# Performance work log

Hardware: AMD Instinct MI355X
Metric: run time of the kernel (lower is better)

The kernel has to match this reference:

```python
import jax, jax.numpy as jnp
import numpy as np

N = 50000      # nodes
E = 400000     # edges
IN = 128       # in_channels
C = 32         # out_channels per head
H1 = 8         # heads layer 1
MSG = 64       # msg_dim
TD = 64        # time encoder out_channels
ED = MSG + TD  # edge_dim = 128
HID = H1 * C   # 256


def _lin(k, fi, fo):
    return jax.random.normal(k, (fi, fo), jnp.float32) / np.float32(np.sqrt(fi))


def setup_inputs() -> dict:
    key = jax.random.key(0)
    ks = jax.random.split(key, 32)
    inp = {
        'x': jax.random.normal(ks[0], (N, IN), jnp.float32),
        'last_update': jax.random.uniform(ks[1], (N,), jnp.float32) * 1000.0,
        'edge_index': jax.random.randint(ks[2], (2, E), 0, N, jnp.int64),
        't': jax.random.uniform(ks[3], (E,), jnp.float32) * 1000.0,
        'msg': jax.random.normal(ks[4], (E, MSG), jnp.float32),
        # time encoder: Linear(1, TD) then cos
        'tw': jax.random.normal(ks[5], (TD,), jnp.float32),
        'tb': jnp.zeros((TD,), jnp.float32),
        # layer 1: TransformerConv(IN, C, heads=8, concat=True, edge_dim=ED)
        'Wq1': _lin(ks[6], IN, HID), 'bq1': jnp.zeros((HID,), jnp.float32),
        'Wk1': _lin(ks[7], IN, HID), 'bk1': jnp.zeros((HID,), jnp.float32),
        'Wv1': _lin(ks[8], IN, HID), 'bv1': jnp.zeros((HID,), jnp.float32),
        'We1': _lin(ks[9], ED, HID),                       # lin_edge, no bias
        'Ws1': _lin(ks[10], IN, HID), 'bs1': jnp.zeros((HID,), jnp.float32),
        # layer 2: TransformerConv(HID, C, heads=1, concat=False, edge_dim=ED)
        'Wq2': _lin(ks[11], HID, C), 'bq2': jnp.zeros((C,), jnp.float32),
        'Wk2': _lin(ks[12], HID, C), 'bk2': jnp.zeros((C,), jnp.float32),
        'Wv2': _lin(ks[13], HID, C), 'bv2': jnp.zeros((C,), jnp.float32),
        'We2': _lin(ks[14], ED, C),
        'Ws2': _lin(ks[15], HID, C), 'bs2': jnp.zeros((C,), jnp.float32),
    }
    return inp


def _seg_softmax(logits, seg, n):
    # numerically-stable softmax over variable-size neighborhoods (per dst node)
    m = jax.ops.segment_max(logits, seg, num_segments=n)
    m = jnp.where(jnp.isfinite(m), m, 0.0)
    e = jnp.exp(logits - jax.lax.stop_gradient(m)[seg])
    s = jax.ops.segment_sum(e, seg, num_segments=n)
    return e / (s[seg] + 1e-16)


def _transformer_conv(x, edge_attr, src, dst, Wq, bq, Wk, bk, Wv, bv, We, Ws, bs, heads, ch, concat):
    n = x.shape[0]
    q = (x @ Wq + bq).reshape(n, heads, ch)[dst]          # (E,H,C) gather at dst
    k = ((x @ Wk + bk)[src]).reshape(-1, heads, ch)       # (E,H,C) gather at src
    v = ((x @ Wv + bv)[src]).reshape(-1, heads, ch)
    e = (edge_attr @ We).reshape(-1, heads, ch)
    k = k + e
    alpha = (q * k).sum(-1) / np.float32(np.sqrt(ch))     # (E,H)
    alpha = _seg_softmax(alpha, dst, n)
    out = jax.ops.segment_sum(alpha[..., None] * (v + e), dst, num_segments=n)  # (N,H,C)
    out = out.reshape(n, heads * ch) if concat else out.mean(axis=1)
    return out + x @ Ws + bs                               # root/skip connection


def reference(x, last_update, edge_index, t, msg, tw, tb,
              Wq1, bq1, Wk1, bk1, Wv1, bv1, We1, Ws1, bs1,
              Wq2, bq2, Wk2, bk2, Wv2, bv2, We2, Ws2, bs2):
    src, dst = edge_index[0], edge_index[1]
    rel_t = last_update[src] - t                          # (E,)
    rel_enc = jnp.cos(rel_t[:, None] * tw[None, :] + tb)  # TGN time encoding (E,TD)
    edge_attr = jnp.concatenate([rel_enc, msg], axis=-1)  # (E,ED)
    h = jax.nn.relu(_transformer_conv(x, edge_attr, src, dst,
                                      Wq1, bq1, Wk1, bk1, Wv1, bv1, We1, Ws1, bs1,
                                      H1, C, True))
    out = jax.nn.relu(_transformer_conv(h, edge_attr, src, dst,
                                        Wq2, bq2, Wk2, bk2, Wv2, bv2, We2, Ws2, bs2,
                                        1, C, False))
    return out
```

## Files before the change

kernel.cpp:

```cpp
#include <hip/hip_runtime.h>
#include <math.h>

#define NN 50000
#define NE 400000
#define RSQRT32 0.17677669529663687f

typedef __attribute__((ext_vector_type(8))) short bf16x8;
typedef __attribute__((ext_vector_type(4))) float f32x4;
#define MFMA_B16(a, b, c) __builtin_amdgcn_mfma_f32_16x16x32_bf16(a, b, c, 0, 0, 0)

#define O_FLAG  0ULL
#define O_BSUM  256ULL
#define O_SRCI  1280ULL
#define O_DSTI  (O_SRCI + 1600000ULL)
#define O_DEG   (O_DSTI + 1600000ULL)
#define O_CUR   (O_DEG + 200192ULL)
#define O_START (O_CUR + 200192ULL)
#define O_SRCS  (O_START + 200704ULL)
#define O_ORIG  (O_SRCS + 1600000ULL)
#define O_RELT  (O_ORIG + 1600000ULL)
#define O_Q1    (O_RELT + 1600000ULL)
#define O_K1    (O_Q1 + 25600000ULL)
#define O_V1    (O_K1 + 25600000ULL)
#define O_S1M   (O_V1 + 25600000ULL)
#define O_G1    (O_S1M + 25600000ULL)
#define O_WB1   (O_G1 + 102400000ULL)
#define O_WG1   (O_WB1 + 262144ULL)
#define O_WF1   (O_WG1 + 65536ULL)
#define O_WB2   (O_WF1 + 65536ULL)
#define O_NUMV1 (O_WB2 + 65536ULL)
#define WS_TOTAL (O_NUMV1 + 51200000ULL)
#define O_S1    O_DSTI
#define O_A1    O_G1
#define O_H     O_V1
#define O_Q2    O_Q1
#define O_K2    (O_Q1 + 6400000ULL)
#define O_V2    (O_Q1 + 12800000ULL)
#define O_S2M   (O_Q1 + 19200000ULL)
#define O_G2    O_K1
#define O_A2    O_S1M
#define O_NUMV2 O_G1
#define O_S2    O_CUR

__device__ __forceinline__ unsigned short f2bf(float f) {
    unsigned int u = __float_as_uint(f);
    unsigned int r = (u + 0x7fffu + ((u >> 16) & 1u)) >> 16;
    return (unsigned short)r;
}
__device__ __forceinline__ float bf2f(unsigned short u) {
    return __uint_as_float(((unsigned int)u) << 16);
}
__device__ __forceinline__ float4 ld_bf16x4(const unsigned short* p) {
    const ushort4 u = *(const ushort4*)p;
    float4 r;
    r.x = bf2f(u.x); r.y = bf2f(u.y); r.z = bf2f(u.z); r.w = bf2f(u.w);
    return r;
}
__device__ __forceinline__ ushort4 st_bf16x4(float a, float b, float c, float d) {
    ushort4 u; u.x = f2bf(a); u.y = f2bf(b); u.z = f2bf(c); u.w = f2bf(d);
    return u;
}

__global__ void k_detect(const unsigned int* ei, int* flag) {
    if (threadIdx.x == 0) {
        int is64 = 1;
        for (int i = 0; i < 64; ++i)
            if (ei[2 * i + 1] != 0u) { is64 = 0; break; }
        *flag = is64;
    }
}

__global__ void k_convhist(const void* ei, const int* flag,
                           int* __restrict__ srcI, int* __restrict__ dstI,
                           int* __restrict__ deg) {
    int i = blockIdx.x * 256 + threadIdx.x;
    if (i >= NE) return;
    int s, d;
    if (*flag) {
        const long long* p = (const long long*)ei;
        s = (int)p[i]; d = (int)p[NE + i];
    } else {
        const int* p = (const int*)ei;
        s = p[i]; d = p[NE + i];
    }
    srcI[i] = s;
    dstI[i] = d;
    atomicAdd(&deg[d], 1);
}

__global__ void k_scanA(const int* __restrict__ deg, int* __restrict__ locs,
                        int* __restrict__ bsum) {
    __shared__ int sm[256];
    const int t = threadIdx.x;
    const int gidx = blockIdx.x * 256 + t;
    int v = (gidx < NN) ? deg[gidx] : 0;
    sm[t] = v;
    __syncthreads();
    for (int off = 1; off < 256; off <<= 1) {
        int u = (t >= off) ? sm[t - off] : 0;
        __syncthreads();
        sm[t] += u;
        __syncthreads();
    }
    if (gidx < NN) locs[gidx] = sm[t];
    if (t == 255) bsum[blockIdx.x] = sm[255];
}

__global__ void k_scanB(int* __restrict__ bsum) {
    __shared__ int sm[256];
    const int t = threadIdx.x;
    int v = (t < 196) ? bsum[t] : 0;
    sm[t] = v;
    __syncthreads();
    for (int off = 1; off < 256; off <<= 1) {
        int u = (t >= off) ? sm[t - off] : 0;
        __syncthreads();
        sm[t] += u;
        __syncthreads();
    }
    if (t < 196) bsum[t] = sm[t] - v;
}

__global__ void k_scanC(const int* __restrict__ deg, const int* __restrict__ bsum,
                        int* __restrict__ startA, int* __restrict__ cursor) {
    const int t = threadIdx.x;
    const int gidx = blockIdx.x * 256 + t;
    if (gidx < NN) {
        const int ex = startA[gidx] - deg[gidx] + bsum[blockIdx.x];
        startA[gidx] = ex;
        cursor[gidx] = ex;
    }
    if (gidx == 0) startA[NN] = NE;
}

__global__ void k_scatter(const int* __restrict__ srcI, const int* __restrict__ dstI,
                          const float* __restrict__ lu, const float* __restrict__ tE,
                          int* __restrict__ cursor,
                          int* __restrict__ srcS, int* __restrict__ orig,
                          float* __restrict__ relT) {
    int i = blockIdx.x * 256 + threadIdx.x;
    if (i >= NE) return;
    const int d = dstI[i];
    const int s = srcI[i];
    const int pos = atomicAdd(&cursor[d], 1);
    srcS[pos] = s;
    orig[pos] = i;
    relT[pos] = lu[s] - tE[i];
}

__global__ void k_prepw(
    const float* __restrict__ Wq1, const float* __restrict__ Wk1,
    const float* __restrict__ Wv1, const float* __restrict__ Ws1,
    const float* __restrict__ We1,
    const float* __restrict__ Wq2, const float* __restrict__ Wk2,
    const float* __restrict__ Wv2, const float* __restrict__ Ws2,
    unsigned short* __restrict__ WB1, unsigned short* __restrict__ WG1,
    unsigned short* __restrict__ WF1, unsigned short* __restrict__ WB2)
{
    const int i = blockIdx.x * 256 + threadIdx.x;
    if (i < 131072) {
        const int part = i >> 15;
        const int rem = i & 32767;
        const int n = rem >> 7, k = rem & 127;
        const float* W = part == 0 ? Wq1 : part == 1 ? Wk1 : part == 2 ? Wv1 : Ws1;
        WB1[i] = f2bf(W[(size_t)k * 256 + n]);
    } else if (i < 163840) {
        const int j = i - 131072;
        const int h = j >> 12, ko = (j >> 5) & 127, c = j & 31;
        WG1[j] = f2bf(We1[(size_t)ko * 256 + h * 32 + c]);
    } else if (i < 196608) {
        const int j = i - 163840;
        const int h = j >> 12, c = (j >> 7) & 31, ko = j & 127;
        WF1[j] = f2bf(We1[(size_t)ko * 256 + h * 32 + c]);
    } else if (i < 229376) {
        const int j = i - 196608;
        const int col = j >> 8, k = j & 255;
        const int part = col >> 5, pc = col & 31;
        const float* W = part == 0 ? Wq2 : part == 1 ? Wk2 : part == 2 ? Wv2 : Ws2;
        WB2[j] = f2bf(W[(size_t)k * 32 + pc]);
    }
}

__global__ __launch_bounds__(256) void k_gemm1m(
    const float* __restrict__ x, const unsigned short* __restrict__ WB1,
    const float* __restrict__ c0, const float* __restrict__ c1,
    const float* __restrict__ c2, const float* __restrict__ c3,
    unsigned short* __restrict__ Q1b, unsigned short* __restrict__ K1b,
    unsigned short* __restrict__ V1b, unsigned short* __restrict__ S1mb)
{
    __shared__ unsigned short As[64 * 136];
    __shared__ unsigned short Bs[64 * 136];
    const int t = threadIdx.x;
    const int row0 = blockIdx.x * 64;
    const int by = blockIdx.y;
    const int part = by >> 2;
    const int pcol0 = (by & 3) * 64;
    const float* bp = part == 0 ? c0 : part == 1 ? c1 : part == 2 ? c2 : c3;
    unsigned short* Ob = part == 0 ? Q1b : part == 1 ? K1b : part == 2 ? V1b : S1mb;

    {
        const int r = t >> 2, cc = (t & 3) * 32;
        const int gr = row0 + r;
        unsigned short* dst = As + r * 136 + cc;
        if (gr < NN) {
            const float4* xp = (const float4*)(x + (size_t)gr * 128 + cc);
            #pragma unroll
            for (int i = 0; i < 8; ++i) {
                const float4 v = xp[i];
                *(ushort4*)(dst + 4 * i) = st_bf16x4(v.x, v.y, v.z, v.w);
            }
        } else {
            const ushort4 z = {0, 0, 0, 0};
            #pragma unroll
            for (int i = 0; i < 8; ++i) *(ushort4*)(dst + 4 * i) = z;
        }
    }
    {
        const int n = t >> 2, kk = (t & 3) * 32;
        const unsigned short* src = WB1 + ((size_t)part * 256 + pcol0 + n) * 128 + kk;
        unsigned short* dst = Bs + n * 136 + kk;
        #pragma unroll
        for (int i = 0; i < 4; ++i)
            *(bf16x8*)(dst + 8 * i) = *(const bf16x8*)(src + 8 * i);
    }
    __syncthreads();

    const int w = t >> 6, lane = t & 63, m = lane & 15, quad = lane >> 4;
    f32x4 acc[4];
    #pragma unroll
    for (int i = 0; i < 4; ++i) acc[i] = (f32x4){0.f, 0.f, 0.f, 0.f};
    #pragma unroll
    for (int kc = 0; kc < 4; ++kc) {
        const bf16x8 af = *(const bf16x8*)(As + (16 * w + m) * 136 + kc * 32 + quad * 8);
        #pragma unroll
        for (int ct = 0; ct < 4; ++ct) {
            const bf16x8 bf = *(const bf16x8*)(Bs + (16 * ct + m) * 136 + kc * 32 + quad * 8);
            acc[ct] = MFMA_B16(af, bf, acc[ct]);
        }
    }
    #pragma unroll
    for (int ct = 0; ct < 4; ++ct) {
        const int colp = pcol0 + ct * 16 + m;
        const float b = bp[colp];
        #pragma unroll
        for (int r = 0; r < 4; ++r) {
            const int gr = row0 + 16 * w + quad * 4 + r;
            if (gr < NN) Ob[(size_t)gr * 256 + colp] = f2bf(acc[ct][r] + b);
        }
    }
}

__global__ __launch_bounds__(256) void k_g1m(
    const unsigned short* __restrict__ Q1b, const unsigned short* __restrict__ WG1,
    unsigned short* __restrict__ G1b)
{
    __shared__ unsigned short As[64 * 40];
    __shared__ unsigned short Bs[128 * 40];
    const int t = threadIdx.x;
    const int n0 = blockIdx.x * 64;
    const int h = blockIdx.y;
    {
        const int n = t >> 2, c = (t & 3) * 8;
        const int gn = n0 + n;
        bf16x8 v = {};
        if (gn < NN) v = *(const bf16x8*)(Q1b + (size_t)gn * 256 + h * 32 + c);
        *(bf16x8*)(As + n * 40 + c) = v;
    }
    {
        const int ko = t >> 1, c = (t & 1) * 16;
        const unsigned short* src = WG1 + (size_t)h * 4096 + ko * 32 + c;
        *(bf16x8*)(Bs + ko * 40 + c) = *(const bf16x8*)(src);
        *(bf16x8*)(Bs + ko * 40 + c + 8) = *(const bf16x8*)(src + 8);
    }
    __syncthreads();

    const int w = t >> 6, lane = t & 63, m = lane & 15, quad = lane >> 4;
    f32x4 acc[8];
    #pragma unroll
    for (int i = 0; i < 8; ++i) acc[i] = (f32x4){0.f, 0.f, 0.f, 0.f};
    const bf16x8 af = *(const bf16x8*)(As + (16 * w + m) * 40 + quad * 8);
    #pragma unroll
    for (int ct = 0; ct < 8; ++ct) {
        const bf16x8 bf = *(const bf16x8*)(Bs + (16 * ct + m) * 40 + quad * 8);
        acc[ct] = MFMA_B16(af, bf, acc[ct]);
    }
    #pragma unroll
    for (int ct = 0; ct < 8; ++ct) {
        const int k = ct * 16 + m;
        #pragma unroll
        for (int r = 0; r < 4; ++r) {
            const int gn = n0 + 16 * w + quad * 4 + r;
            if (gn < NN) G1b[(size_t)gn * 1024 + h * 128 + k] = f2bf(acc[ct][r]);
        }
    }
}

__global__ __launch_bounds__(256) void k_g2(
    const float* __restrict__ Q2, const float* __restrict__ We2,
    float* __restrict__ G2)
{
    __shared__ float Qs[64][36];
    __shared__ float Ws[128][36];
    const int t = threadIdx.x;
    const int n0 = blockIdx.x * 64;
    {
        const int n = t >> 2, c8 = (t & 3) * 8;
        float4 v0 = make_float4(0.f,0.f,0.f,0.f), v1 = v0;
        if (n0 + n < NN) {
            v0 = *(const float4*)(Q2 + (size_t)(n0 + n) * 32 + c8);
            v1 = *(const float4*)(Q2 + (size_t)(n0 + n) * 32 + c8 + 4);
        }
        *(float4*)(&Qs[n][c8]) = v0;
        *(float4*)(&Qs[n][c8 + 4]) = v1;
    }
    {
        const int k = t >> 1, c16 = (t & 1) * 16;
        #pragma unroll
        for (int i = 0; i < 4; ++i)
            *(float4*)(&Ws[k][c16 + 4 * i]) =
                *(const float4*)(We2 + (size_t)k * 32 + c16 + 4 * i);
    }
    __syncthreads();
    const int tx = t & 15, ty = t >> 4;
    const int k8 = tx * 8, n4 = ty * 4;
    float acc[4][8] = {};
    #pragma unroll 8
    for (int c = 0; c < 32; ++c) {
        float a[4], b[8];
        #pragma unroll
        for (int i = 0; i < 4; ++i) a[i] = Qs[n4 + i][c];
        #pragma unroll
        for (int j = 0; j < 8; ++j) b[j] = Ws[k8 + j][c];
        #pragma unroll
        for (int i = 0; i < 4; ++i)
            #pragma unroll
            for (int j = 0; j < 8; ++j)
                acc[i][j] += a[i] * b[j];
    }
    #pragma unroll
    for (int i = 0; i < 4; ++i) {
        const int gn = n0 + n4 + i;
        if (gn < NN) {
            float* gp = G2 + (size_t)gn * 128 + k8;
            *(float4*)(gp)     = make_float4(acc[i][0], acc[i][1], acc[i][2], acc[i][3]);
            *(float4*)(gp + 4) = make_float4(acc[i][4], acc[i][5], acc[i][6], acc[i][7]);
        }
    }
}

__global__ __launch_bounds__(256, 4) void k_agg1(
    const int* __restrict__ startA, const int* __restrict__ srcS,
    const int* __restrict__ orig, const float* __restrict__ relT,
    const float* __restrict__ msg, const float* __restrict__ tw,
    const float* __restrict__ tb,
    const unsigned short* __restrict__ Q1b, const unsigned short* __restrict__ K1b,
    const unsigned short* __restrict__ V1b, const unsigned short* G1b,
    unsigned short* A1b, float* __restrict__ numv1, float* __restrict__ s1)
{
    const int t = threadIdx.x;
    const int g = t >> 5, l = t & 31;
    const int lane64 = t & 63;
    const int d = blockIdx.x * 8 + g;
    const int eb = startA[d], ee = startA[d + 1];
    const int hl = l >> 2;

    float q8[8];
    {
        const unsigned short* qp = Q1b + (size_t)d * 256 + l * 8;
        const float4 q0 = ld_bf16x4(qp), q1 = ld_bf16x4(qp + 4);
        q8[0]=q0.x; q8[1]=q0.y; q8[2]=q0.z; q8[3]=q0.w;
        q8[4]=q1.x; q8[5]=q1.y; q8[6]=q1.z; q8[7]=q1.w;
    }
    float gv[8][4];
    #pragma unroll
    for (int h = 0; h < 8; ++h) {
        const float4 gg = ld_bf16x4(G1b + (size_t)d * 1024 + h * 128 + l * 4);
        gv[h][0]=gg.x; gv[h][1]=gg.y; gv[h][2]=gg.z; gv[h][3]=gg.w;
    }
    float4 twl = make_float4(0.f,0.f,0.f,0.f), tbl = twl;
    if (l < 16) {
        twl = *(const float4*)(tw + l * 4);
        tbl = *(const float4*)(tb + l * 4);
    }

    float a1acc[8][4] = {};
    float nv[8] = {};
    float sacc = 0.f;

    for (int e = eb; e < ee; ++e) {
        const int s = srcS[e];
        float a[4];
        if (l < 16) {
            const float rt = relT[e];
            a[0] = __cosf(rt * twl.x + tbl.x);
            a[1] = __cosf(rt * twl.y + tbl.y);
            a[2] = __cosf(rt * twl.z + tbl.z);
            a[3] = __cosf(rt * twl.w + tbl.w);
        } else {
            const float4 m4 = *(const float4*)(msg + (size_t)orig[e] * 64 + (l - 16) * 4);
            a[0]=m4.x; a[1]=m4.y; a[2]=m4.z; a[3]=m4.w;
        }
        float part[8];
        #pragma unroll
        for (int h = 0; h < 8; ++h)
            part[h] = a[0]*gv[h][0] + a[1]*gv[h][1] + a[2]*gv[h][2] + a[3]*gv[h][3];
        {
            const unsigned short* kp = K1b + (size_t)s * 256 + l * 8;
            const float4 k0 = ld_bf16x4(kp), k1 = ld_bf16x4(kp + 4);
            part[hl] += q8[0]*k0.x + q8[1]*k0.y + q8[2]*k0.z + q8[3]*k0.w
                      + q8[4]*k1.x + q8[5]*k1.y + q8[6]*k1.z + q8[7]*k1.w;
        }
        #pragma unroll
        for (int mk = 1; mk < 32; mk <<= 1) {
            #pragma unroll
            for (int h = 0; h < 8; ++h)
                part[h] += __shfl_xor(part[h], mk);
        }
        const float pe = __expf(fminf(part[lane64 & 7] * RSQRT32, 80.f));
        float p_all[8];
        #pragma unroll
        for (int h = 0; h < 8; ++h)
            p_all[h] = __shfl(pe, (lane64 & 32) + h);
        #pragma unroll
        for (int h = 0; h < 8; ++h) {
            a1acc[h][0] += p_all[h]*a[0]; a1acc[h][1] += p_all[h]*a[1];
            a1acc[h][2] += p_all[h]*a[2]; a1acc[h][3] += p_all[h]*a[3];
        }
        {
            const unsigned short* vp = V1b + (size_t)s * 256 + l * 8;
            const float4 v0 = ld_bf16x4(vp), v1 = ld_bf16x4(vp + 4);
            const float pv = p_all[hl];
            nv[0] += pv*v0.x; nv[1] += pv*v0.y; nv[2] += pv*v0.z; nv[3] += pv*v0.w;
            nv[4] += pv*v1.x; nv[5] += pv*v1.y; nv[6] += pv*v1.z; nv[7] += pv*v1.w;
            sacc += pv;
        }
    }
    #pragma unroll
    for (int h = 0; h < 8; ++h)
        *(ushort4*)(A1b + (size_t)d * 1024 + h * 128 + l * 4) =
            st_bf16x4(a1acc[h][0], a1acc[h][1], a1acc[h][2], a1acc[h][3]);
    float* np = numv1 + (size_t)d * 256 + l * 8;
    *(float4*)(np)     = make_float4(nv[0], nv[1], nv[2], nv[3]);
    *(float4*)(np + 4) = make_float4(nv[4], nv[5], nv[6], nv[7]);
    if ((l & 3) == 0) s1[(size_t)d * 8 + hl] = sacc;
}

__global__ __launch_bounds__(256) void k_foldC1m(
    const unsigned short* __restrict__ A1b, const unsigned short* __restrict__ WF1,
    const float* __restrict__ numv1, const float* __restrict__ s1,
    const unsigned short* __restrict__ S1mb, unsigned short* __restrict__ hb)
{
    __shared__ unsigned short As[64 * 136];
    __shared__ unsigned short Bs[32 * 136];
    const int t = threadIdx.x;
    const int n0 = blockIdx.x * 64;
    const int h = blockIdx.y;
    {
        const int n = t >> 2, kk = (t & 3) * 32;
        const int gn = n0 + n;
        unsigned short* dst = As + n * 136 + kk;
        if (gn < NN) {
            const unsigned short* src = A1b + (size_t)gn * 1024 + h * 128 + kk;
            #pragma unroll
            for (int i = 0; i < 4; ++i)
                *(bf16x8*)(dst + 8 * i) = *(const bf16x8*)(src + 8 * i);
        } else {
            const bf16x8 z = {};
            #pragma unroll
            for (int i = 0; i < 4; ++i) *(bf16x8*)(dst + 8 * i) = z;
        }
    }
    {
        const int c = t >> 3, kk = (t & 7) * 16;
        const unsigned short* src = WF1 + (size_t)h * 4096 + c * 128 + kk;
        *(bf16x8*)(Bs + c * 136 + kk) = *(const bf16x8*)(src);
        *(bf16x8*)(Bs + c * 136 + kk + 8) = *(const bf16x8*)(src + 8);
    }
    __syncthreads();

    const int w = t >> 6, lane = t & 63, m = lane & 15, quad = lane >> 4;
    f32x4 acc[2];
    acc[0] = (f32x4){0.f, 0.f, 0.f, 0.f};
    acc[1] = (f32x4){0.f, 0.f, 0.f, 0.f};
    #pragma unroll
    for (int kc = 0; kc < 4; ++kc) {
        const bf16x8 af = *(const bf16x8*)(As + (16 * w + m) * 136 + kc * 32 + quad * 8);
        #pragma unroll
        for (int ct = 0; ct < 2; ++ct) {
            const bf16x8 bf = *(const bf16x8*)(Bs + (16 * ct + m) * 136 + kc * 32 + quad * 8);
            acc[ct] = MFMA_B16(af, bf, acc[ct]);
        }
    }
    #pragma unroll
    for (int ct = 0; ct < 2; ++ct) {
        const int c = ct * 16 + m;
        #pragma unroll
        for (int r = 0; r < 4; ++r) {
            const int gn = n0 + 16 * w + quad * 4 + r;
            if (gn < NN) {
                const float s = s1[(size_t)gn * 8 + h] + 1e-16f;
                const float nvv = numv1[(size_t)gn * 256 + h * 32 + c];
                const float sk = bf2f(S1mb[(size_t)gn * 256 + h * 32 + c]);
                float v = (acc[ct][r] + nvv) / s + sk;
                v = v > 0.f ? v : 0.f;
                hb[(size_t)gn * 256 + h * 32 + c] = f2bf(v);
            }
        }
    }
}

__global__ __launch_bounds__(256) void k_gemm2m(
    const unsigned short* __restrict__ hb, const unsigned short* __restrict__ WB2,
    const float* __restrict__ c0, const float* __restrict__ c1,
    const float* __restrict__ c2, const float* __restrict__ c3,
    float* __restrict__ O0, float* __restrict__ O1,
    float* __restrict__ O2, float* __restrict__ O3)
{
    __shared__ unsigned short As[64 * 136];
    __shared__ unsigned short Bs[64 * 136];
    const int t = threadIdx.x;
    const int row0 = blockIdx.x * 64;
    const int coly = blockIdx.y;
    const int w = t >> 6, lane = t & 63, m = lane & 15, quad = lane >> 4;

    f32x4 acc[4];
    #pragma unroll
    for (int i = 0; i < 4; ++i) acc[i] = (f32x4){0.f, 0.f, 0.f, 0.f};

    for (int kb = 0; kb < 2; ++kb) {
        if (kb) __syncthreads();
        {
            const int r = t >> 2, kk = (t & 3) * 32;
            const int gr = row0 + r;
            unsigned short* dst = As + r * 136 + kk;
            if (gr < NN) {
                const unsigned short* src = hb + (size_t)gr * 256 + kb * 128 + kk;
                #pragma unroll
                for (int i = 0; i < 4; ++i)
                    *(bf16x8*)(dst + 8 * i) = *(const bf16x8*)(src + 8 * i);
            } else {
                const bf16x8 z = {};
                #pragma unroll
                for (int i = 0; i < 4; ++i) *(bf16x8*)(dst + 8 * i) = z;
            }
        }
        {
            const int n = t >> 2, kk = (t & 3) * 32;
            const unsigned short* src = WB2 + (size_t)(coly * 64 + n) * 256 + kb * 128 + kk;
            unsigned short* dst = Bs + n * 136 + kk;
            #pragma unroll
            for (int i = 0; i < 4; ++i)
                *(bf16x8*)(dst + 8 * i) = *(const bf16x8*)(src + 8 * i);
        }
        __syncthreads();
        #pragma unroll
        for (int kc = 0; kc < 4; ++kc) {
            const bf16x8 af = *(const bf16x8*)(As + (16 * w + m) * 136 + kc * 32 + quad * 8);
            #pragma unroll
            for (int ct = 0; ct < 4; ++ct) {
                const bf16x8 bf = *(const bf16x8*)(Bs + (16 * ct + m) * 136 + kc * 32 + quad * 8);
                acc[ct] = MFMA_B16(af, bf, acc[ct]);
            }
        }
    }
    #pragma unroll
    for (int ct = 0; ct < 4; ++ct) {
        const int col = coly * 64 + ct * 16 + m;
        const int part = col >> 5, pc = col & 31;
        const float* bb = part == 0 ? c0 : part == 1 ? c1 : part == 2 ? c2 : c3;
        float* Op = part == 0 ? O0 : part == 1 ? O1 : part == 2 ? O2 : O3;
        const float b = bb[pc];
        #pragma unroll
        for (int r = 0; r < 4; ++r) {
            const int gr = row0 + 16 * w + quad * 4 + r;
            if (gr < NN) Op[(size_t)gr * 32 + pc] = acc[ct][r] + b;
        }
    }
}

__global__ __launch_bounds__(256) void k_aggB2(
    const int* __restrict__ startA, const int* __restrict__ srcS,
    const int* __restrict__ orig, const float* __restrict__ relT,
    const float* __restrict__ msg, const float* __restrict__ tw,
    const float* __restrict__ tb,
    const float* __restrict__ Q2, const float* __restrict__ K2,
    const float* __restrict__ V2, const float* __restrict__ G2,
    float* __restrict__ A2, float* __restrict__ numv2, float* __restrict__ s2)
{
    const int t = threadIdx.x;
    const int g = t >> 5, l = t & 31;
    const int d = blockIdx.x * 8 + g;
    const int eb = startA[d], ee = startA[d + 1];

    const float q2l = Q2[(size_t)d * 32 + l];
    const float4 g2l = *(const float4*)(G2 + (size_t)d * 128 + l * 4);
    float4 twl = make_float4(0.f,0.f,0.f,0.f), tbl = twl;
    if (l < 16) {
        twl = *(const float4*)(tw + l * 4);
        tbl = *(const float4*)(tb + l * 4);
    }
    float acc2[4] = {};
    float nvacc = 0.f, sacc = 0.f;

    for (int e = eb; e < ee; ++e) {
        const int s = srcS[e];
        float a[4];
        if (l < 16) {
            const float rt = relT[e];
            a[0] = __cosf(rt * twl.x + tbl.x);
            a[1] = __cosf(rt * twl.y + tbl.y);
            a[2] = __cosf(rt * twl.z + tbl.z);
            a[3] = __cosf(rt * twl.w + tbl.w);
        } else {
            const float4 m4 = *(const float4*)(msg + (size_t)orig[e] * 64 + (l - 16) * 4);
            a[0] = m4.x; a[1] = m4.y; a[2] = m4.z; a[3] = m4.w;
        }
        float part = q2l * K2[(size_t)s * 32 + l];
        part += a[0] * g2l.x + a[1] * g2l.y + a[2] * g2l.z + a[3] * g2l.w;
        part += __shfl_xor(part, 1);
        part += __shfl_xor(part, 2);
        part += __shfl_xor(part, 4);
        part += __shfl_xor(part, 8);
        part += __shfl_xor(part, 16);
        const float p = __expf(fminf(part * RSQRT32, 80.f));
        acc2[0] += p * a[0]; acc2[1] += p * a[1];
        acc2[2] += p * a[2]; acc2[3] += p * a[3];
        nvacc += p * V2[(size_t)s * 32 + l];
        sacc += p;
    }
    *(float4*)(A2 + (size_t)d * 128 + l * 4) =
        make_float4(acc2[0], acc2[1], acc2[2], acc2[3]);
    numv2[(size_t)d * 32 + l] = nvacc;
    if (l == 0) s2[d] = sacc;
}

__global__ __launch_bounds__(256) void k_foldC2(
    const float* __restrict__ A2, const float* __restrict__ We2,
    const float* __restrict__ numv2, const float* __restrict__ s2,
    const float* __restrict__ S2m, float* __restrict__ out)
{
    __shared__ float Ws[128][36];
    const int t = threadIdx.x;
    {
        const int k = t >> 1, c16 = (t & 1) * 16;
        #pragma unroll
        for (int i = 0; i < 4; ++i)
            *(float4*)(&Ws[k][c16 + 4 * i]) =
                *(const float4*)(We2 + (size_t)k * 32 + c16 + 4 * i);
    }
    __syncthreads();
    const int n = blockIdx.x * 8 + (t >> 5);
    const int c = t & 31;
    const float* ap = A2 + (size_t)n * 128;
    float acc = 0.f;
    #pragma unroll 8
    for (int k = 0; k < 128; k += 4) {
        const float4 a4 = *(const float4*)(ap + k);
        acc += a4.x * Ws[k][c] + a4.y * Ws[k + 1][c] +
               a4.z * Ws[k + 2][c] + a4.w * Ws[k + 3][c];
    }
    const float s = s2[n] + 1e-16f;
    float v = (numv2[(size_t)n * 32 + c] + acc) / s + S2m[(size_t)n * 32 + c];
    out[(size_t)n * 32 + c] = v > 0.f ? v : 0.f;
}

extern "C" void kernel_launch(void* const* d_in, const int* in_sizes, int n_in,
                              void* d_out, int out_size, void* d_ws, size_t ws_size,
                              hipStream_t stream) {
    const float* x   = (const float*)d_in[0];
    const float* lu  = (const float*)d_in[1];
    const void*  ei  = d_in[2];
    const float* tE  = (const float*)d_in[3];
    const float* msg = (const float*)d_in[4];
    const float* tw  = (const float*)d_in[5];
    const float* tb  = (const float*)d_in[6];
    const float* Wq1 = (const float*)d_in[7];  const float* bq1 = (const float*)d_in[8];
    const float* Wk1 = (const float*)d_in[9];  const float* bk1 = (const float*)d_in[10];
    const float* Wv1 = (const float*)d_in[11]; const float* bv1 = (const float*)d_in[12];
    const float* We1 = (const float*)d_in[13];
    const float* Ws1 = (const float*)d_in[14]; const float* bs1 = (const float*)d_in[15];
    const float* Wq2 = (const float*)d_in[16]; const float* bq2 = (const float*)d_in[17];
    const float* Wk2 = (const float*)d_in[18]; const float* bk2 = (const float*)d_in[19];
    const float* Wv2 = (const float*)d_in[20]; const float* bv2 = (const float*)d_in[21];
    const float* We2 = (const float*)d_in[22];
    const float* Ws2 = (const float*)d_in[23]; const float* bs2 = (const float*)d_in[24];
    float* out = (float*)d_out;
    char* ws = (char*)d_ws;

    if (ws_size < WS_TOTAL) return;

    int* flag   = (int*)(ws + O_FLAG);
    int* bsum   = (int*)(ws + O_BSUM);
    int* srcI   = (int*)(ws + O_SRCI);
    int* dstI   = (int*)(ws + O_DSTI);
    int* deg    = (int*)(ws + O_DEG);
    int* cursor = (int*)(ws + O_CUR);
    int* startA = (int*)(ws + O_START);
    int* srcS   = (int*)(ws + O_SRCS);
    int* orig   = (int*)(ws + O_ORIG);
    float* relT = (float*)(ws + O_RELT);
    unsigned short* Q1b  = (unsigned short*)(ws + O_Q1);
    unsigned short* K1b  = (unsigned short*)(ws + O_K1);
    unsigned short* V1b  = (unsigned short*)(ws + O_V1);
    unsigned short* S1mb = (unsigned short*)(ws + O_S1M);
    unsigned short* G1b  = (unsigned short*)(ws + O_G1);
    unsigned short* A1b  = (unsigned short*)(ws + O_A1);
    float* numv1 = (float*)(ws + O_NUMV1);
    float* s1    = (float*)(ws + O_S1);
    unsigned short* hb = (unsigned short*)(ws + O_H);
    float* Q2   = (float*)(ws + O_Q2);
    float* K2m  = (float*)(ws + O_K2);
    float* V2m  = (float*)(ws + O_V2);
    float* S2m  = (float*)(ws + O_S2M);
    float* G2   = (float*)(ws + O_G2);
    float* A2   = (float*)(ws + O_A2);
    float* numv2 = (float*)(ws + O_NUMV2);
    float* s2   = (float*)(ws + O_S2);
    unsigned short* WB1 = (unsigned short*)(ws + O_WB1);
    unsigned short* WG1 = (unsigned short*)(ws + O_WG1);
    unsigned short* WF1 = (unsigned short*)(ws + O_WF1);
    unsigned short* WB2 = (unsigned short*)(ws + O_WB2);

    hipMemsetAsync(ws + O_DEG, 0, 200000, stream);

    k_detect<<<1, 64, 0, stream>>>((const unsigned int*)ei, flag);
    k_convhist<<<(NE + 255) / 256, 256, 0, stream>>>(ei, flag, srcI, dstI, deg);
    k_scanA<<<196, 256, 0, stream>>>(deg, startA, bsum);
    k_scanB<<<1, 256, 0, stream>>>(bsum);
    k_scanC<<<196, 256, 0, stream>>>(deg, bsum, startA, cursor);
    k_scatter<<<(NE + 255) / 256, 256, 0, stream>>>(srcI, dstI, lu, tE, cursor,
                                                    srcS, orig, relT);
    k_prepw<<<896, 256, 0, stream>>>(Wq1, Wk1, Wv1, Ws1, We1, Wq2, Wk2, Wv2, Ws2,
                                     WB1, WG1, WF1, WB2);
    k_gemm1m<<<dim3(782, 16), 256, 0, stream>>>(
        x, WB1, bq1, bk1, bv1, bs1, Q1b, K1b, V1b, S1mb);
    k_g1m<<<dim3(782, 8), 256, 0, stream>>>(Q1b, WG1, G1b);
    k_agg1<<<NN / 8, 256, 0, stream>>>(startA, srcS, orig, relT, msg, tw, tb,
                                       Q1b, K1b, V1b, G1b, A1b, numv1, s1);
    k_foldC1m<<<dim3(782, 8), 256, 0, stream>>>(A1b, WF1, numv1, s1, S1mb, hb);
    k_gemm2m<<<dim3(782, 2), 256, 0, stream>>>(
        hb, WB2, bq2, bk2, bv2, bs2, Q2, K2m, V2m, S2m);
    k_g2<<<782, 256, 0, stream>>>(Q2, We2, G2);
    k_aggB2<<<NN / 8, 256, 0, stream>>>(startA, srcS, orig, relT, msg, tw, tb,
                                        Q2, K2m, V2m, G2, A2, numv2, s2);
    k_foldC2<<<NN / 8, 256, 0, stream>>>(A2, We2, numv2, s2, S2m, out);
}
```

Baseline: 860.0 us.

## Prefetch next edge's gathers and use transpose-reduce for per-head logits

Both aggregation kernels now software-pipeline the per-edge loop. They issue the next edge's source index, K/V row gathers, message load and cosine time encoding before computing the current edge, so gather latency overlaps with arithmetic. In layer 1, the 8-head butterfly all-reduce (40 shuffles) is replaced by a recursive-halving transpose reduction (about 9 shuffles) that leaves one head's sum per lane. The exp-broadcast lane indices are permuted to match that layout. This raises register pressure from holding prefetched data, and the launch bounds of 4 blocks per SM could cause spills.

```diff
diff --git a/kernel.cpp b/kernel.cpp
--- a/kernel.cpp
+++ b/kernel.cpp
@@ -360,6 +360,7 @@
     const int t = threadIdx.x;
     const int g = t >> 5, l = t & 31;
     const int lane64 = t & 63;
+    const int base32 = lane64 & 32;
     const int d = blockIdx.x * 8 + g;
     const int eb = startA[d], ee = startA[d + 1];
     const int hl = l >> 2;
@@ -387,54 +388,106 @@
     float nv[8] = {};
     float sacc = 0.f;
 
+    const unsigned short* kbase = K1b + l * 8;
+    const unsigned short* vbase = V1b + l * 8;
+
+    bf16x8 kN = {}, vN = {};
+    float aN[4] = {0.f, 0.f, 0.f, 0.f};
+
+    #define PREF1(EIDX) {                                                     \
+        const int s_ = srcS[EIDX];                                            \
+        if (l < 16) {                                                         \
+            const float rt_ = relT[EIDX];                                     \
+            aN[0] = __cosf(rt_ * twl.x + tbl.x);                              \
+            aN[1] = __cosf(rt_ * twl.y + tbl.y);                              \
+            aN[2] = __cosf(rt_ * twl.z + tbl.z);                              \
+            aN[3] = __cosf(rt_ * twl.w + tbl.w);                              \
+        } else {                                                              \
+            const float4 m4_ = *(const float4*)(msg + (size_t)orig[EIDX] * 64 \
+                                                + (l - 16) * 4);              \
+            aN[0]=m4_.x; aN[1]=m4_.y; aN[2]=m4_.z; aN[3]=m4_.w;               \
+        }                                                                     \
+        kN = *(const bf16x8*)(kbase + (size_t)s_ * 256);                      \
+        vN = *(const bf16x8*)(vbase + (size_t)s_ * 256);                      \
+    }
+
+    if (eb < ee) PREF1(eb);
+
     for (int e = eb; e < ee; ++e) {
-        const int s = srcS[e];
-        float a[4];
-        if (l < 16) {
-            const float rt = relT[e];
-            a[0] = __cosf(rt * twl.x + tbl.x);
-            a[1] = __cosf(rt * twl.y + tbl.y);
-            a[2] = __cosf(rt * twl.z + tbl.z);
-            a[3] = __cosf(rt * twl.w + tbl.w);
-        } else {
-            const float4 m4 = *(const float4*)(msg + (size_t)orig[e] * 64 + (l - 16) * 4);
-            a[0]=m4.x; a[1]=m4.y; a[2]=m4.z; a[3]=m4.w;
-        }
+        const bf16x8 kc = kN, vc = vN;
+        const float a0 = aN[0], a1 = aN[1], a2 = aN[2], a3 = aN[3];
+        if (e + 1 < ee) PREF1(e + 1);
+
         float part[8];
         #pragma unroll
         for (int h = 0; h < 8; ++h)
-            part[h] = a[0]*gv[h][0] + a[1]*gv[h][1] + a[2]*gv[h][2] + a[3]*gv[h][3];
+            part[h] = a0*gv[h][0] + a1*gv[h][1] + a2*gv[h][2] + a3*gv[h][3];
         {
-            const unsigned short* kp = K1b + (size_t)s * 256 + l * 8;
-            const float4 k0 = ld_bf16x4(kp), k1 = ld_bf16x4(kp + 4);
-            part[hl] += q8[0]*k0.x + q8[1]*k0.y + q8[2]*k0.z + q8[3]*k0.w
-                      + q8[4]*k1.x + q8[5]*k1.y + q8[6]*k1.z + q8[7]*k1.w;
-        }
-        #pragma unroll
-        for (int mk = 1; mk < 32; mk <<= 1) {
-            #pragma unroll
-            for (int h = 0; h < 8; ++h)
-                part[h] += __shfl_xor(part[h], mk);
-        }
-        const float pe = __expf(fminf(part[lane64 & 7] * RSQRT32, 80.f));
+            float kf[8];
+            #pragma unroll
+            for (int i = 0; i < 8; ++i) kf[i] = bf2f((unsigned short)kc[i]);
+            part[hl] += q8[0]*kf[0] + q8[1]*kf[1] + q8[2]*kf[2] + q8[3]*kf[3]
+                      + q8[4]*kf[4] + q8[5]*kf[5] + q8[6]*kf[6] + q8[7]*kf[7];
+        }
+
+        float t4[4];
+        {
+            const bool b = (l & 1) != 0;
+            #pragma unroll
+            for (int i = 0; i < 4; ++i) {
+                const float give = b ? part[i] : part[4 + i];
+                const float keep = b ? part[4 + i] : part[i];
+                t4[i] = keep + __shfl_xor(give, 1);
+            }
+        }
+        float t2[2];
+        {
+            const bool b = (l & 2) != 0;
+            #pragma unroll
+            for (int i = 0; i < 2; ++i) {
+                const float give = b ? t4[i] : t4[2 + i];
+                const float keep = b ? t4[2 + i] : t4[i];
+                t2[i] = keep + __shfl_xor(give, 2);
+            }
+        }
+        float t1;
+        {
+            const bool b = (l & 4) != 0;
+            const float give = b ? t2[0] : t2[1];
+            const float keep = b ? t2[1] : t2[0];
+            t1 = keep + __shfl_xor(give, 4);
+        }
+        t1 += __shfl_xor(t1, 8);
+        t1 += __shfl_xor(t1, 16);
+
+        const float pe = __expf(fminf(t1 * RSQRT32, 80.f));
         float p_all[8];
-        #pragma unroll
-        for (int h = 0; h < 8; ++h)
-            p_all[h] = __shfl(pe, (lane64 & 32) + h);
+        p_all[0] = __shfl(pe, base32 + 0);
+        p_all[1] = __shfl(pe, base32 + 4);
+        p_all[2] = __shfl(pe, base32 + 2);
+        p_all[3] = __shfl(pe, base32 + 6);
+        p_all[4] = __shfl(pe, base32 + 1);
+        p_all[5] = __shfl(pe, base32 + 5);
+        p_all[6] = __shfl(pe, base32 + 3);
+        p_all[7] = __shfl(pe, base32 + 7);
+
         #pragma unroll
         for (int h = 0; h < 8; ++h) {
-            a1acc[h][0] += p_all[h]*a[0]; a1acc[h][1] += p_all[h]*a[1];
-            a1acc[h][2] += p_all[h]*a[2]; a1acc[h][3] += p_all[h]*a[3];
+            a1acc[h][0] += p_all[h]*a0; a1acc[h][1] += p_all[h]*a1;
+            a1acc[h][2] += p_all[h]*a2; a1acc[h][3] += p_all[h]*a3;
         }
         {
-            const unsigned short* vp = V1b + (size_t)s * 256 + l * 8;
-            const float4 v0 = ld_bf16x4(vp), v1 = ld_bf16x4(vp + 4);
+            float vf[8];
+            #pragma unroll
+            for (int i = 0; i < 8; ++i) vf[i] = bf2f((unsigned short)vc[i]);
             const float pv = p_all[hl];
-            nv[0] += pv*v0.x; nv[1] += pv*v0.y; nv[2] += pv*v0.z; nv[3] += pv*v0.w;
-            nv[4] += pv*v1.x; nv[5] += pv*v1.y; nv[6] += pv*v1.z; nv[7] += pv*v1.w;
+            nv[0] += pv*vf[0]; nv[1] += pv*vf[1]; nv[2] += pv*vf[2]; nv[3] += pv*vf[3];
+            nv[4] += pv*vf[4]; nv[5] += pv*vf[5]; nv[6] += pv*vf[6]; nv[7] += pv*vf[7];
             sacc += pv;
         }
     }
+    #undef PREF1
+
     #pragma unroll
     for (int h = 0; h < 8; ++h)
         *(ushort4*)(A1b + (size_t)d * 1024 + h * 128 + l * 4) =
@@ -602,32 +655,48 @@
     float acc2[4] = {};
     float nvacc = 0.f, sacc = 0.f;
 
+    float kNv = 0.f, vNv = 0.f;
+    float aN[4] = {0.f, 0.f, 0.f, 0.f};
+
+    #define PREF2(EIDX) {                                                     \
+        const int s_ = srcS[EIDX];                                            \
+        kNv = K2[(size_t)s_ * 32 + l];                                        \
+        vNv = V2[(size_t)s_ * 32 + l];                                        \
+        if (l < 16) {                                                         \
+            const float rt_ = relT[EIDX];                                     \
+            aN[0] = __cosf(rt_ * twl.x + tbl.x);                              \
+            aN[1] = __cosf(rt_ * twl.y + tbl.y);                              \
+            aN[2] = __cosf(rt_ * twl.z + tbl.z);                              \
+            aN[3] = __cosf(rt_ * twl.w + tbl.w);                              \
+        } else {                                                              \
+            const float4 m4_ = *(const float4*)(msg + (size_t)orig[EIDX] * 64 \
+                                                + (l - 16) * 4);              \
+            aN[0]=m4_.x; aN[1]=m4_.y; aN[2]=m4_.z; aN[3]=m4_.w;               \
+        }                                                                     \
+    }
+
+    if (eb < ee) PREF2(eb);
+
     for (int e = eb; e < ee; ++e) {
-        const int s = srcS[e];
-        float a[4];
-        if (l < 16) {
-            const float rt = relT[e];
-            a[0] = __cosf(rt * twl.x + tbl.x);
-            a[1] = __cosf(rt * twl.y + tbl.y);
-            a[2] = __cosf(rt * twl.z + tbl.z);
-            a[3] = __cosf(rt * twl.w + tbl.w);
-        } else {
-            const float4 m4 = *(const float4*)(msg + (size_t)orig[e] * 64 + (l - 16) * 4);
-            a[0] = m4.x; a[1] = m4.y; a[2] = m4.z; a[3] = m4.w;
-        }
-        float part = q2l * K2[(size_t)s * 32 + l];
-        part += a[0] * g2l.x + a[1] * g2l.y + a[2] * g2l.z + a[3] * g2l.w;
+        const float kc = kNv, vcv = vNv;
+        const float a0 = aN[0], a1 = aN[1], a2 = aN[2], a3 = aN[3];
+        if (e + 1 < ee) PREF2(e + 1);
+
+        float part = q2l * kc;
+        part += a0 * g2l.x + a1 * g2l.y + a2 * g2l.z + a3 * g2l.w;
         part += __shfl_xor(part, 1);
         part += __shfl_xor(part, 2);
         part += __shfl_xor(part, 4);
         part += __shfl_xor(part, 8);
         part += __shfl_xor(part, 16);
         const float p = __expf(fminf(part * RSQRT32, 80.f));
-        acc2[0] += p * a[0]; acc2[1] += p * a[1];
-        acc2[2] += p * a[2]; acc2[3] += p * a[3];
-        nvacc += p * V2[(size_t)s * 32 + l];
+        acc2[0] += p * a0; acc2[1] += p * a1;
+        acc2[2] += p * a2; acc2[3] += p * a3;
+        nvacc += p * vcv;
         sacc += p;
     }
+    #undef PREF2
+
     *(float4*)(A2 + (size_t)d * 128 + l * 4) =
         make_float4(acc2[0], acc2[1], acc2[2], acc2[3]);
     numv2[(size_t)d * 32 + l] = nvacc;
```

After: 977.3 us. +13.6%, slower.

## Software-pipeline edge gathers in aggregation kernels and use a transpose-reduce for head sums

Applied to the files above, without the earlier changes.

Both edge-aggregation kernels now load up to 32 edge indices, relative times and original ids cooperatively, one per lane, then broadcast them with shuffles. K/V/msg gathers are issued two edges ahead through a double buffer, hiding the latency of dependent global loads. In layer 1, the 8-head butterfly reduction (40 shuffles) is replaced by a recursive halving transpose-reduce (about 9 shuffles), and the waves-per-EU hint is changed. The cost is higher register pressure, which may lower occupancy.

```diff
diff --git a/kernel.cpp b/kernel.cpp
--- a/kernel.cpp
+++ b/kernel.cpp
@@ -348,7 +348,96 @@
     }
 }
 
-__global__ __launch_bounds__(256, 4) void k_agg1(
+#define AGG1_ISSUE(S, JJ)                                                     \
+    {                                                                         \
+        const int s_ = __shfl(sv, base32 + (JJ));                             \
+        rS##S = __shfl(rv, base32 + (JJ));                                    \
+        const int o_ = __shfl(ov, base32 + (JJ));                             \
+        kS##S = *(const bf16x8*)(kbase + (size_t)s_ * 256);                   \
+        vS##S = *(const bf16x8*)(vbase + (size_t)s_ * 256);                   \
+        if (l >= 16)                                                          \
+            mS##S = *(const float4*)(msg + (size_t)o_ * 64 + (l - 16) * 4);   \
+    }
+
+#define AGG1_BODY(KC, VC, MC, RC)                                             \
+    {                                                                         \
+        float a0_, a1_, a2_, a3_;                                             \
+        if (l < 16) {                                                         \
+            a0_ = __cosf((RC) * twl.x + tbl.x);                               \
+            a1_ = __cosf((RC) * twl.y + tbl.y);                               \
+            a2_ = __cosf((RC) * twl.z + tbl.z);                               \
+            a3_ = __cosf((RC) * twl.w + tbl.w);                               \
+        } else {                                                              \
+            a0_ = (MC).x; a1_ = (MC).y; a2_ = (MC).z; a3_ = (MC).w;           \
+        }                                                                     \
+        float part[8];                                                        \
+        _Pragma("unroll")                                                     \
+        for (int h = 0; h < 8; ++h)                                           \
+            part[h] = a0_*gv[h][0] + a1_*gv[h][1] + a2_*gv[h][2] + a3_*gv[h][3]; \
+        {                                                                     \
+            float kf[8];                                                      \
+            _Pragma("unroll")                                                 \
+            for (int i = 0; i < 8; ++i) kf[i] = bf2f((unsigned short)(KC)[i]); \
+            part[hl] += q8[0]*kf[0] + q8[1]*kf[1] + q8[2]*kf[2] + q8[3]*kf[3] \
+                      + q8[4]*kf[4] + q8[5]*kf[5] + q8[6]*kf[6] + q8[7]*kf[7]; \
+        }                                                                     \
+        float t4[4];                                                          \
+        {                                                                     \
+            const bool b_ = (l & 1) != 0;                                     \
+            _Pragma("unroll")                                                 \
+            for (int i = 0; i < 4; ++i) {                                     \
+                const float give = b_ ? part[i] : part[4 + i];                \
+                const float keep = b_ ? part[4 + i] : part[i];                \
+                t4[i] = keep + __shfl_xor(give, 1);                           \
+            }                                                                 \
+        }                                                                     \
+        float t2[2];                                                          \
+        {                                                                     \
+            const bool b_ = (l & 2) != 0;                                     \
+            _Pragma("unroll")                                                 \
+            for (int i = 0; i < 2; ++i) {                                     \
+                const float give = b_ ? t4[i] : t4[2 + i];                    \
+                const float keep = b_ ? t4[2 + i] : t4[i];                    \
+                t2[i] = keep + __shfl_xor(give, 2);                           \
+            }                                                                 \
+        }                                                                     \
+        float t1;                                                             \
+        {                                                                     \
+            const bool b_ = (l & 4) != 0;                                     \
+            const float give = b_ ? t2[0] : t2[1];                            \
+            const float keep = b_ ? t2[1] : t2[0];                            \
+            t1 = keep + __shfl_xor(give, 4);                                  \
+        }                                                                     \
+        t1 += __shfl_xor(t1, 8);                                              \
+        t1 += __shfl_xor(t1, 16);                                             \
+        const float pe = __expf(fminf(t1 * RSQRT32, 80.f));                   \
+        float p_all[8];                                                       \
+        p_all[0] = __shfl(pe, base32 + 0);                                    \
+        p_all[1] = __shfl(pe, base32 + 4);                                    \
+        p_all[2] = __shfl(pe, base32 + 2);                                    \
+        p_all[3] = __shfl(pe, base32 + 6);                                    \
+        p_all[4] = __shfl(pe, base32 + 1);                                    \
+        p_all[5] = __shfl(pe, base32 + 5);                                    \
+        p_all[6] = __shfl(pe, base32 + 3);                                    \
+        p_all[7] = __shfl(pe, base32 + 7);                                    \
+        _Pragma("unroll")                                                     \
+        for (int h = 0; h < 8; ++h) {                                         \
+            a1acc[h][0] += p_all[h]*a0_; a1acc[h][1] += p_all[h]*a1_;         \
+            a1acc[h][2] += p_all[h]*a2_; a1acc[h][3] += p_all[h]*a3_;         \
+        }                                                                     \
+        {                                                                     \
+            float vf[8];                                                      \
+            _Pragma("unroll")                                                 \
+            for (int i = 0; i < 8; ++i) vf[i] = bf2f((unsigned short)(VC)[i]); \
+            const float pv = p_all[hl];                                       \
+            nv[0] += pv*vf[0]; nv[1] += pv*vf[1]; nv[2] += pv*vf[2]; nv[3] += pv*vf[3]; \
+            nv[4] += pv*vf[4]; nv[5] += pv*vf[5]; nv[6] += pv*vf[6]; nv[7] += pv*vf[7]; \
+            sacc += pv;                                                       \
+        }                                                                     \
+    }
+
+__global__ __launch_bounds__(256) __attribute__((amdgpu_waves_per_eu(3)))
+void k_agg1(
     const int* __restrict__ startA, const int* __restrict__ srcS,
     const int* __restrict__ orig, const float* __restrict__ relT,
     const float* __restrict__ msg, const float* __restrict__ tw,
@@ -359,7 +448,7 @@
 {
     const int t = threadIdx.x;
     const int g = t >> 5, l = t & 31;
-    const int lane64 = t & 63;
+    const int base32 = (t & 63) & 32;
     const int d = blockIdx.x * 8 + g;
     const int eb = startA[d], ee = startA[d + 1];
     const int hl = l >> 2;
@@ -387,54 +476,40 @@
     float nv[8] = {};
     float sacc = 0.f;
 
-    for (int e = eb; e < ee; ++e) {
-        const int s = srcS[e];
-        float a[4];
-        if (l < 16) {
-            const float rt = relT[e];
-            a[0] = __cosf(rt * twl.x + tbl.x);
-            a[1] = __cosf(rt * twl.y + tbl.y);
-            a[2] = __cosf(rt * twl.z + tbl.z);
-            a[3] = __cosf(rt * twl.w + tbl.w);
-        } else {
-            const float4 m4 = *(const float4*)(msg + (size_t)orig[e] * 64 + (l - 16) * 4);
-            a[0]=m4.x; a[1]=m4.y; a[2]=m4.z; a[3]=m4.w;
-        }
-        float part[8];
-        #pragma unroll
-        for (int h = 0; h < 8; ++h)
-            part[h] = a[0]*gv[h][0] + a[1]*gv[h][1] + a[2]*gv[h][2] + a[3]*gv[h][3];
-        {
-            const unsigned short* kp = K1b + (size_t)s * 256 + l * 8;
-            const float4 k0 = ld_bf16x4(kp), k1 = ld_bf16x4(kp + 4);
-            part[hl] += q8[0]*k0.x + q8[1]*k0.y + q8[2]*k0.z + q8[3]*k0.w
-                      + q8[4]*k1.x + q8[5]*k1.y + q8[6]*k1.z + q8[7]*k1.w;
-        }
-        #pragma unroll
-        for (int mk = 1; mk < 32; mk <<= 1) {
-            #pragma unroll
-            for (int h = 0; h < 8; ++h)
-                part[h] += __shfl_xor(part[h], mk);
-        }
-        const float pe = __expf(fminf(part[lane64 & 7] * RSQRT32, 80.f));
-        float p_all[8];
-        #pragma unroll
-        for (int h = 0; h < 8; ++h)
-            p_all[h] = __shfl(pe, (lane64 & 32) + h);
-        #pragma unroll
-        for (int h = 0; h < 8; ++h) {
-            a1acc[h][0] += p_all[h]*a[0]; a1acc[h][1] += p_all[h]*a[1];
-            a1acc[h][2] += p_all[h]*a[2]; a1acc[h][3] += p_all[h]*a[3];
-        }
-        {
-            const unsigned short* vp = V1b + (size_t)s * 256 + l * 8;
-            const float4 v0 = ld_bf16x4(vp), v1 = ld_bf16x4(vp + 4);
-            const float pv = p_all[hl];
-            nv[0] += pv*v0.x; nv[1] += pv*v0.y; nv[2] += pv*v0.z; nv[3] += pv*v0.w;
-            nv[4] += pv*v1.x; nv[5] += pv*v1.y; nv[6] += pv*v1.z; nv[7] += pv*v1.w;
-            sacc += pv;
-        }
-    }
+    const unsigned short* kbase = K1b + l * 8;
+    const unsigned short* vbase = V1b + l * 8;
+
+    for (int c = eb; c < ee; c += 32) {
+        const int cnt = (ee - c < 32) ? (ee - c) : 32;
+        const bool lvld = (c + l) < ee;
+        const int   sv = lvld ? srcS[c + l] : 0;
+        const float rv = lvld ? relT[c + l] : 0.f;
+        const int   ov = lvld ? orig[c + l] : 0;
+
+        bf16x8 kS0 = {}, vS0 = {}, kS1 = {}, vS1 = {};
+        float4 mS0 = make_float4(0.f,0.f,0.f,0.f), mS1 = mS0;
+        float  rS0 = 0.f, rS1 = 0.f;
+
+        AGG1_ISSUE(0, 0);
+        if (cnt > 1) AGG1_ISSUE(1, 1);
+        for (int j = 0; j < cnt; j += 2) {
+            {
+                const bf16x8 kc_ = kS0, vc_ = vS0;
+                const float4 mc_ = mS0;
+                const float  rc_ = rS0;
+                if (j + 2 < cnt) AGG1_ISSUE(0, j + 2);
+                AGG1_BODY(kc_, vc_, mc_, rc_)
+            }
+            if (j + 1 < cnt) {
+                const bf16x8 kc_ = kS1, vc_ = vS1;
+                const float4 mc_ = mS1;
+                const float  rc_ = rS1;
+                if (j + 3 < cnt) AGG1_ISSUE(1, j + 3);
+                AGG1_BODY(kc_, vc_, mc_, rc_)
+            }
+        }
+    }
+
     #pragma unroll
     for (int h = 0; h < 8; ++h)
         *(ushort4*)(A1b + (size_t)d * 1024 + h * 128 + l * 4) =
@@ -578,7 +653,44 @@
     }
 }
 
-__global__ __launch_bounds__(256) void k_aggB2(
+#define AGG2_ISSUE(S, JJ)                                                     \
+    {                                                                         \
+        const int s_ = __shfl(sv, base32 + (JJ));                             \
+        rS##S = __shfl(rv, base32 + (JJ));                                    \
+        const int o_ = __shfl(ov, base32 + (JJ));                             \
+        kS##S = K2[(size_t)s_ * 32 + l];                                      \
+        vS##S = V2[(size_t)s_ * 32 + l];                                      \
+        if (l >= 16)                                                          \
+            mS##S = *(const float4*)(msg + (size_t)o_ * 64 + (l - 16) * 4);   \
+    }
+
+#define AGG2_BODY(KC, VC, MC, RC)                                             \
+    {                                                                         \
+        float a0_, a1_, a2_, a3_;                                             \
+        if (l < 16) {                                                         \
+            a0_ = __cosf((RC) * twl.x + tbl.x);                               \
+            a1_ = __cosf((RC) * twl.y + tbl.y);                               \
+            a2_ = __cosf((RC) * twl.z + tbl.z);                               \
+            a3_ = __cosf((RC) * twl.w + tbl.w);                               \
+        } else {                                                              \
+            a0_ = (MC).x; a1_ = (MC).y; a2_ = (MC).z; a3_ = (MC).w;           \
+        }                                                                     \
+        float part = q2l * (KC);                                              \
+        part += a0_ * g2l.x + a1_ * g2l.y + a2_ * g2l.z + a3_ * g2l.w;        \
+        part += __shfl_xor(part, 1);                                          \
+        part += __shfl_xor(part, 2);                                          \
+        part += __shfl_xor(part, 4);                                          \
+        part += __shfl_xor(part, 8);                                          \
+        part += __shfl_xor(part, 16);                                         \
+        const float p = __expf(fminf(part * RSQRT32, 80.f));                  \
+        acc2[0] += p * a0_; acc2[1] += p * a1_;                               \
+        acc2[2] += p * a2_; acc2[3] += p * a3_;                               \
+        nvacc += p * (VC);                                                    \
+        sacc += p;                                                            \
+    }
+
+__global__ __launch_bounds__(256) __attribute__((amdgpu_waves_per_eu(4)))
+void k_aggB2(
     const int* __restrict__ startA, const int* __restrict__ srcS,
     const int* __restrict__ orig, const float* __restrict__ relT,
     const float* __restrict__ msg, const float* __restrict__ tw,
@@ -589,6 +701,7 @@
 {
     const int t = threadIdx.x;
     const int g = t >> 5, l = t & 31;
+    const int base32 = (t & 63) & 32;
     const int d = blockIdx.x * 8 + g;
     const int eb = startA[d], ee = startA[d + 1];
 
@@ -602,32 +715,37 @@
     float acc2[4] = {};
     float nvacc = 0.f, sacc = 0.f;
 
-    for (int e = eb; e < ee; ++e) {
-        const int s = srcS[e];
-        float a[4];
-        if (l < 16) {
-            const float rt = relT[e];
-            a[0] = __cosf(rt * twl.x + tbl.x);
-            a[1] = __cosf(rt * twl.y + tbl.y);
-            a[2] = __cosf(rt * twl.z + tbl.z);
-            a[3] = __cosf(rt * twl.w + tbl.w);
-        } else {
-            const float4 m4 = *(const float4*)(msg + (size_t)orig[e] * 64 + (l - 16) * 4);
-            a[0] = m4.x; a[1] = m4.y; a[2] = m4.z; a[3] = m4.w;
-        }
-        float part = q2l * K2[(size_t)s * 32 + l];
-        part += a[0] * g2l.x + a[1] * g2l.y + a[2] * g2l.z + a[3] * g2l.w;
-        part += __shfl_xor(part, 1);
-        part += __shfl_xor(part, 2);
-        part += __shfl_xor(part, 4);
-        part += __shfl_xor(part, 8);
-        part += __shfl_xor(part, 16);
-        const float p = __expf(fminf(part * RSQRT32, 80.f));
-        acc2[0] += p * a[0]; acc2[1] += p * a[1];
-        acc2[2] += p * a[2]; acc2[3] += p * a[3];
-        nvacc += p * V2[(size_t)s * 32 + l];
-        sacc += p;
-    }
+    for (int c = eb; c < ee; c += 32) {
+        const int cnt = (ee - c < 32) ? (ee - c) : 32;
+        const bool lvld = (c + l) < ee;
+        const int   sv = lvld ? srcS[c + l] : 0;
+        const float rv = lvld ? relT[c + l] : 0.f;
+        const int   ov = lvld ? orig[c + l] : 0;
+
+        float kS0 = 0.f, vS0 = 0.f, kS1 = 0.f, vS1 = 0.f;
+        float rS0 = 0.f, rS1 = 0.f;
+        float4 mS0 = make_float4(0.f,0.f,0.f,0.f), mS1 = mS0;
+
+        AGG2_ISSUE(0, 0);
+        if (cnt > 1) AGG2_ISSUE(1, 1);
+        for (int j = 0; j < cnt; j += 2) {
+            {
+                const float kc_ = kS0, vc_ = vS0;
+                const float4 mc_ = mS0;
+                const float  rc_ = rS0;
+                if (j + 2 < cnt) AGG2_ISSUE(0, j + 2);
+                AGG2_BODY(kc_, vc_, mc_, rc_)
+            }
+            if (j + 1 < cnt) {
+                const float kc_ = kS1, vc_ = vS1;
+                const float4 mc_ = mS1;
+                const float  rc_ = rS1;
+                if (j + 3 < cnt) AGG2_ISSUE(1, j + 3);
+                AGG2_BODY(kc_, vc_, mc_, rc_)
+            }
+        }
+    }
+
     *(float4*)(A2 + (size_t)d * 128 + l * 4) =
         make_float4(acc2[0], acc2[1], acc2[2], acc2[3]);
     numv2[(size_t)d * 32 + l] = nvacc;
```

Result: faster. 742.2 us (-13.7%).
